# Kernel optimization log

Hardware: AMD Instinct MI355X
Metric: run time of the kernel (lower is better)

The kernel has to match this reference:

```python
import jax, jax.numpy as jnp
import numpy as np

B, N, D, H, CH = 16, 2048, 2, 128, 32
NEG = -1e9


def setup_inputs() -> dict:
    key = jax.random.key(0)
    ks = jax.random.split(key, 24)
    u = lambda k, shape, fan_in: jax.random.uniform(k, shape, jnp.float32,
                                                    -1.0 / np.sqrt(fan_in), 1.0 / np.sqrt(fan_in))
    inp = {
        "features": jax.random.normal(ks[0], (B, N, D), jnp.float32),
        "adj": jax.random.randint(ks[1], (B, N, N), 0, 2, jnp.int32),
        "candidates": jax.random.randint(ks[2], (B, N), 0, 2, jnp.int32).at[:, 0].set(1),
        "action": jnp.zeros((B,), jnp.int32),
        # GCN encoder (3 layers)
        "W1": u(ks[3], (D, H), D), "b1": jnp.zeros((H,), jnp.float32),
        "W2": u(ks[4], (H, H), H), "b2": jnp.zeros((H,), jnp.float32),
        "W3": u(ks[5], (H, H), H), "b3": jnp.zeros((H,), jnp.float32),
        # learned machine state
        "machine_state": jax.random.uniform(ks[6], (H,), jnp.float32, -1.0, 1.0),
        # actor MLP: Linear(3H,H) -> ReLU -> Linear(H,H) -> ReLU -> Linear(H,1)
        "A1": u(ks[7], (3 * H, H), 3 * H), "ab1": u(ks[8], (H,), 3 * H),
        "A2": u(ks[9], (H, H), H), "ab2": u(ks[10], (H,), H),
        "A3": u(ks[11], (H, 1), H), "ab3": u(ks[12], (1,), H),
        # critic MLP: Linear(H,CH) -> ReLU -> Linear(CH,1)
        "C1": u(ks[13], (H, CH), H), "cb1": u(ks[14], (CH,), H),
        "C2": u(ks[15], (CH, 1), CH), "cb2": u(ks[16], (1,), CH),
    }
    return inp


def _gcn_propagation_matrix(adj):
    # Faithful to PyG GCNConv(add_self_loops=True) fed edges from dense_to_sparse
    # with edge attrs discarded (all weights 1).
    A = (adj != 0).astype(jnp.float32)                      # (B,N,N), A[b,j,i]: edge j->i
    A = jnp.maximum(A, jnp.eye(N, dtype=jnp.float32))       # add_remaining_self_loops
    deg = A.sum(axis=1)                                     # (B,N) incoming degree per target i
    dis = jax.lax.rsqrt(deg)                                # deg >= 1 due to self loops
    # S[b,j,i] = dis[j] * A[j,i] * dis[i]
    return dis[:, :, None] * A * dis[:, None, :]


def reference(features, adj, candidates, action,
              W1, b1, W2, b2, W3, b3, machine_state,
              A1, ab1, A2, ab2, A3, ab3, C1, cb1, C2, cb2):
    S = _gcn_propagation_matrix(adj)
    h = features
    for W, b in ((W1, b1), (W2, b2), (W3, b3)):
        # out[b,i,:] = sum_j S[b,j,i] * (h W)[b,j,:]
        h = jax.nn.relu(jnp.einsum('bji,bjd->bid', S, h @ W) + b)
    pool = h.mean(axis=1)                                   # (B,H) global mean pool

    concat = jnp.concatenate(
        [h,
         jnp.broadcast_to(pool[:, None, :], h.shape),
         jnp.broadcast_to(machine_state[None, None, :], h.shape)], axis=-1)  # (B,N,3H)
    a = jax.nn.relu(concat @ A1 + ab1)
    a = jax.nn.relu(a @ A2 + ab2)
    scores = ((a @ A3 + ab3)[..., 0]) * 10.0                # (B,N)

    probs_sm = jax.nn.softmax(scores, axis=1)               # softmax over jobs
    logits = jnp.where(candidates != 0, probs_sm, NEG)      # masked_fill(~candidates, -inf)
    logp = jax.nn.log_softmax(logits, axis=1)               # Categorical(logits=...)
    log_prob = jnp.take_along_axis(logp, action[:, None].astype(jnp.int32), axis=1)[:, 0]
    p = jnp.exp(logp)
    entropy = -(p * logp).sum(axis=1)

    value = jax.nn.relu(pool @ C1 + cb1) @ C2 + cb2         # (B,1)
    return action, log_prob, entropy, value
```

## Files before the change

### kernel.cpp

```cpp
#include <hip/hip_runtime.h>
#include <hip/hip_bf16.h>
#include <stdint.h>

#define B_  16
#define N_  2048
#define D_  2
#define H_  128
#define CH_ 32
#define NEG_ (-1e9f)

typedef __attribute__((ext_vector_type(8))) short bf16x8;
typedef __attribute__((ext_vector_type(4))) float f32x4;
typedef unsigned short u16;

__device__ inline u16 f2bf(float f){
    union { __hip_bfloat16 h; u16 u; } cv;
    cv.h = __float2bfloat16(f);
    return cv.u;
}
__device__ inline float bf2f(u16 v){ return __uint_as_float(((unsigned)v) << 16); }

__device__ inline void gld16(const u16* g, u16* l){
    __builtin_amdgcn_global_load_lds(
        (const __attribute__((address_space(1))) unsigned int*)(const void*)g,
        (__attribute__((address_space(3))) unsigned int*)(void*)l, 16, 0, 0);
}

__global__ __launch_bounds__(256) void k_prep(const int* __restrict__ adj,
                                              u16* __restrict__ ATbf,
                                              float* __restrict__ degF){
    int i0 = blockIdx.x * 64, j0 = blockIdx.y * 64, b = blockIdx.z;
    __shared__ u16 tile[64 * 72];
    __shared__ float degP[256];
    int t = threadIdx.x;
    const int* ap = adj + (size_t)b * N_ * N_;
    #pragma unroll
    for (int it = 0; it < 4; ++it){
        int jj = it * 16 + (t >> 4);
        int gi0 = (t & 15) * 4;
        int4 a4 = *(const int4*)&ap[(size_t)(j0 + jj) * N_ + i0 + gi0];
        int gj = j0 + jj;
        tile[(gi0 + 0) * 72 + jj] = (a4.x != 0 || gj == i0 + gi0 + 0) ? (u16)0x3F80 : (u16)0;
        tile[(gi0 + 1) * 72 + jj] = (a4.y != 0 || gj == i0 + gi0 + 1) ? (u16)0x3F80 : (u16)0;
        tile[(gi0 + 2) * 72 + jj] = (a4.z != 0 || gj == i0 + gi0 + 2) ? (u16)0x3F80 : (u16)0;
        tile[(gi0 + 3) * 72 + jj] = (a4.w != 0 || gj == i0 + gi0 + 3) ? (u16)0x3F80 : (u16)0;
    }
    __syncthreads();
    {
        int ii = t & 63, q = t >> 6;
        float s = 0.f;
        #pragma unroll
        for (int k = 0; k < 16; ++k) s += (tile[ii * 72 + q * 16 + k] ? 1.f : 0.f);
        degP[t] = s;
    }
    __syncthreads();
    if (t < 64){
        float s = degP[t] + degP[t + 64] + degP[t + 128] + degP[t + 192];
        atomicAdd(&degF[b * N_ + i0 + t], s);
    }
    u16* op = ATbf + (size_t)b * N_ * N_;
    #pragma unroll
    for (int it = 0; it < 2; ++it){
        int idx = it * 256 + t;
        int io = idx >> 3, jo = (idx & 7) * 8;
        *(uint4*)&op[(size_t)(i0 + io) * N_ + j0 + jo] = *(const uint4*)&tile[io * 72 + jo];
    }
}

__global__ __launch_bounds__(256) void k_misc(const float* __restrict__ degF,
                                              float* __restrict__ dis,
                                              const float* __restrict__ W2, u16* __restrict__ WT2,
                                              const float* __restrict__ W3, u16* __restrict__ WT3,
                                              const float* __restrict__ A1, u16* __restrict__ A1aT,
                                              const float* __restrict__ A2, u16* __restrict__ A2T){
    int bx = blockIdx.x;
    if (bx < 128){
        int i = bx * 256 + threadIdx.x;
        dis[i] = rsqrtf(degF[i]);
        return;
    }
    int q = (bx - 128) >> 6;
    const float* s; u16* d;
    switch (q){
        case 0: s = W2; d = WT2; break;
        case 1: s = W3; d = WT3; break;
        case 2: s = A1; d = A1aT; break;
        default: s = A2; d = A2T; break;
    }
    int idx = ((bx - 128) & 63) * 256 + threadIdx.x;
    int hp = idx >> 7, k = idx & 127;
    d[hp * 128 + k] = f2bf(s[k * 128 + hp]);
}

__global__ __launch_bounds__(256) void k_y1(const float* __restrict__ feat,
                                            const float* __restrict__ W1,
                                            const float* __restrict__ dis,
                                            u16* __restrict__ YT){
    int j = blockIdx.x * 256 + threadIdx.x;
    int h = blockIdx.y, b = blockIdx.z;
    float f0 = feat[((size_t)b * N_ + j) * D_ + 0];
    float f1 = feat[((size_t)b * N_ + j) * D_ + 1];
    float v = dis[b * N_ + j] * (f0 * W1[h] + f1 * W1[H_ + h]);
    YT[(size_t)b * H_ * N_ + (size_t)h * N_ + j] = f2bf(v);
}

template<int MODE>
__global__ __launch_bounds__(256, 2) void k_layer(const u16* __restrict__ ATbf,
                                                  const u16* __restrict__ Yin,
                                                  const float* __restrict__ dis,
                                                  const float* __restrict__ bias,
                                                  const u16* __restrict__ WT,
                                                  u16* __restrict__ Yout,
                                                  u16* __restrict__ h3,
                                                  float* __restrict__ poolF){
    int bid = blockIdx.x;
    int b = bid & 15, i0 = (bid >> 4) * 64;
    const u16* Ab = ATbf + (size_t)b * N_ * N_ + (size_t)i0 * N_;
    const u16* Bb = Yin  + (size_t)b * H_ * N_;
    __shared__ __align__(16) u16 As[64 * 64];
    __shared__ __align__(16) u16 Bs[128 * 64];
    __shared__ __align__(16) u16 Hs[64 * 136];
    __shared__ __align__(16) u16 Ws[MODE == 0 ? 128 * 136 : 16];
    int t = threadIdx.x, w = t >> 6, lane = t & 63, quad = lane >> 4, l16 = lane & 15;
    int mr = w & 1, nc = w >> 1;
    int srow = lane >> 3;
    int xcol = ((lane & 7) ^ srow) * 8;
    int x7 = l16 & 7;

    if (MODE == 0){
        #pragma unroll
        for (int it = 0; it < 8; ++it){
            int e = it * 256 + t;
            int row = e >> 4, c8 = e & 15;
            *(uint4*)&Ws[row * 136 + c8 * 8] = *(const uint4*)&WT[row * 128 + c8 * 8];
        }
    }

    f32x4 acc[2][4];
    #pragma unroll
    for (int mt = 0; mt < 2; ++mt)
        #pragma unroll
        for (int nt = 0; nt < 4; ++nt) acc[mt][nt] = (f32x4){0.f, 0.f, 0.f, 0.f};

    for (int k0 = 0; k0 < N_; k0 += 64){
        #pragma unroll
        for (int it = 0; it < 6; ++it){
            int chunk = w * 6 + it;
            if (chunk < 8)
                gld16(Ab + (size_t)(chunk * 8 + srow) * N_ + k0 + xcol, As + chunk * 512);
            else
                gld16(Bb + (size_t)((chunk - 8) * 8 + srow) * N_ + k0 + xcol, Bs + (chunk - 8) * 512);
        }
        __syncthreads();
        #pragma unroll
        for (int kc = 0; kc < 2; ++kc){
            int gx = ((kc * 4 + quad) ^ x7) * 8;
            bf16x8 af[2];
            #pragma unroll
            for (int mt = 0; mt < 2; ++mt)
                af[mt] = *(const bf16x8*)&As[(mr * 32 + mt * 16 + l16) * 64 + gx];
            #pragma unroll
            for (int nt = 0; nt < 4; ++nt){
                bf16x8 bv = *(const bf16x8*)&Bs[(nc * 64 + nt * 16 + l16) * 64 + gx];
                #pragma unroll
                for (int mt = 0; mt < 2; ++mt)
                    acc[mt][nt] = __builtin_amdgcn_mfma_f32_16x16x32_bf16(af[mt], bv, acc[mt][nt], 0, 0, 0);
            }
        }
        __syncthreads();
    }

    #pragma unroll
    for (int mt = 0; mt < 2; ++mt)
        #pragma unroll
        for (int r = 0; r < 4; ++r){
            int m = mr * 32 + mt * 16 + quad * 4 + r;
            float dsc = dis[b * N_ + i0 + m];
            #pragma unroll
            for (int nt = 0; nt < 4; ++nt){
                int n = nc * 64 + nt * 16 + l16;
                float v = dsc * acc[mt][nt][r] + bias[n];
                Hs[m * 136 + n] = f2bf(v > 0.f ? v : 0.f);
            }
        }
    __syncthreads();

    if (MODE == 0){
        f32x4 a2[2][4];
        #pragma unroll
        for (int mt = 0; mt < 2; ++mt)
            #pragma unroll
            for (int nt = 0; nt < 4; ++nt) a2[mt][nt] = (f32x4){0.f, 0.f, 0.f, 0.f};
        #pragma unroll
        for (int kc = 0; kc < 4; ++kc){
            bf16x8 af[2];
            #pragma unroll
            for (int mt = 0; mt < 2; ++mt)
                af[mt] = *(const bf16x8*)&Hs[(mr * 32 + mt * 16 + l16) * 136 + kc * 32 + quad * 8];
            #pragma unroll
            for (int nt = 0; nt < 4; ++nt){
                bf16x8 bv = *(const bf16x8*)&Ws[(nc * 64 + nt * 16 + l16) * 136 + kc * 32 + quad * 8];
                #pragma unroll
                for (int mt = 0; mt < 2; ++mt)
                    a2[mt][nt] = __builtin_amdgcn_mfma_f32_16x16x32_bf16(af[mt], bv, a2[mt][nt], 0, 0, 0);
            }
        }
        __syncthreads();
        #pragma unroll
        for (int mt = 0; mt < 2; ++mt)
            #pragma unroll
            for (int r = 0; r < 4; ++r){
                int m = mr * 32 + mt * 16 + quad * 4 + r;
                float dsc = dis[b * N_ + i0 + m];
                #pragma unroll
                for (int nt = 0; nt < 4; ++nt)
                    Hs[m * 136 + nc * 64 + nt * 16 + l16] = f2bf(dsc * a2[mt][nt][r]);
            }
        __syncthreads();
        size_t obase = (size_t)b * H_ * N_ + i0;
        int j = t & 63, hq = t >> 6;
        #pragma unroll 8
        for (int rep = 0; rep < 32; ++rep){
            int hrow = hq * 32 + rep;
            Yout[obase + (size_t)hrow * N_ + j] = Hs[j * 136 + hrow];
        }
    } else {
        #pragma unroll
        for (int rep = 0; rep < 4; ++rep){
            int e = rep * 256 + t;
            int row = e >> 4, c8 = e & 15;
            *(uint4*)&h3[((size_t)b * N_ + i0 + row) * H_ + c8 * 8] = *(const uint4*)&Hs[row * 136 + c8 * 8];
        }
        __shared__ float pred[256];
        int n = t & 127, rq = t >> 7;
        float ps = 0.f;
        #pragma unroll 8
        for (int r = 0; r < 32; ++r) ps += bf2f(Hs[(rq * 32 + r) * 136 + n]);
        pred[t] = ps;
        __syncthreads();
        if (t < 128)
            atomicAdd(&poolF[b * H_ + t], (pred[t] + pred[t + 128]) * (1.f / N_));
    }
}

__global__ __launch_bounds__(256) void k_cv(const float* __restrict__ poolF,
                                            const float* __restrict__ ms,
                                            const float* __restrict__ A1,
                                            const float* __restrict__ ab1,
                                            const float* __restrict__ C1,
                                            const float* __restrict__ cb1,
                                            const float* __restrict__ C2,
                                            const float* __restrict__ cb2,
                                            float* __restrict__ cvec,
                                            float* __restrict__ out){
    int b = blockIdx.x, t = threadIdx.x;
    __shared__ float pl[128], msl[128], v1[32];
    if (t < 128){ pl[t] = poolF[b * H_ + t]; msl[t] = ms[t]; }
    __syncthreads();
    if (t < 128){
        float c = ab1[t];
        for (int k = 0; k < 128; ++k)
            c += pl[k] * A1[(128 + k) * H_ + t] + msl[k] * A1[(256 + k) * H_ + t];
        cvec[b * H_ + t] = c;
    } else if (t < 160){
        int cc = t - 128;
        float v = cb1[cc];
        for (int k = 0; k < 128; ++k) v += pl[k] * C1[k * CH_ + cc];
        v1[cc] = v > 0.f ? v : 0.f;
    }
    __syncthreads();
    if (t == 0){
        float v = cb2[0];
        for (int c = 0; c < CH_; ++c) v += v1[c] * C2[c];
        out[48 + b] = v;
    }
}

__global__ __launch_bounds__(256) void k_actor(const u16* __restrict__ h3,
                                               const u16* __restrict__ A1aT,
                                               const u16* __restrict__ A2T,
                                               const float* __restrict__ cvec,
                                               const float* __restrict__ ab2,
                                               const float* __restrict__ A3,
                                               const float* __restrict__ ab3,
                                               float* __restrict__ scores){
    int b = blockIdx.x, i0 = blockIdx.y * 128;
    const u16* Ab = h3 + ((size_t)b * N_ + i0) * H_;
    __shared__ __align__(16) u16 As[128 * 72];
    __shared__ __align__(16) u16 Bs[128 * 72];
    __shared__ __align__(16) u16 M1[128 * 136];
    __shared__ float sLDS[128];
    int t = threadIdx.x, w = t >> 6, lane = t & 63, quad = lane >> 4, l16 = lane & 15;
    int sr = t >> 3, sc = (t & 7) * 8;
    f32x4 acc[2][8];
    #pragma unroll
    for (int mt = 0; mt < 2; ++mt)
        #pragma unroll
        for (int nt = 0; nt < 8; ++nt) acc[mt][nt] = (f32x4){0.f, 0.f, 0.f, 0.f};
    for (int k0 = 0; k0 < H_; k0 += 64){
        #pragma unroll
        for (int it = 0; it < 4; ++it){
            int r = sr + it * 32;
            *(uint4*)&As[r * 72 + sc] = *(const uint4*)&Ab[(size_t)r * H_ + k0 + sc];
            *(uint4*)&Bs[r * 72 + sc] = *(const uint4*)&A1aT[(size_t)r * H_ + k0 + sc];
        }
        __syncthreads();
        #pragma unroll
        for (int kc = 0; kc < 2; ++kc){
            bf16x8 af[2];
            #pragma unroll
            for (int mt = 0; mt < 2; ++mt)
                af[mt] = *(const bf16x8*)&As[(w * 32 + mt * 16 + l16) * 72 + kc * 32 + quad * 8];
            #pragma unroll
            for (int nt = 0; nt < 8; ++nt){
                bf16x8 bfr = *(const bf16x8*)&Bs[(nt * 16 + l16) * 72 + kc * 32 + quad * 8];
                #pragma unroll
                for (int mt = 0; mt < 2; ++mt)
                    acc[mt][nt] = __builtin_amdgcn_mfma_f32_16x16x32_bf16(af[mt], bfr, acc[mt][nt], 0, 0, 0);
            }
        }
        __syncthreads();
    }
    const float* cv = cvec + b * H_;
    #pragma unroll
    for (int mt = 0; mt < 2; ++mt)
        #pragma unroll
        for (int r = 0; r < 4; ++r){
            int m = w * 32 + mt * 16 + quad * 4 + r;
            #pragma unroll
            for (int nt = 0; nt < 8; ++nt){
                int n = nt * 16 + l16;
                float v = acc[mt][nt][r] + cv[n];
                M1[m * 136 + n] = f2bf(v > 0.f ? v : 0.f);
                acc[mt][nt][r] = 0.f;
            }
        }
    if (t < 128) sLDS[t] = 0.f;
    for (int k0 = 0; k0 < H_; k0 += 64){
        #pragma unroll
        for (int it = 0; it < 4; ++it){
            int r = sr + it * 32;
            *(uint4*)&Bs[r * 72 + sc] = *(const uint4*)&A2T[(size_t)r * H_ + k0 + sc];
        }
        __syncthreads();
        #pragma unroll
        for (int kc = 0; kc < 2; ++kc){
            bf16x8 af[2];
            #pragma unroll
            for (int mt = 0; mt < 2; ++mt)
                af[mt] = *(const bf16x8*)&M1[(w * 32 + mt * 16 + l16) * 136 + k0 + kc * 32 + quad * 8];
            #pragma unroll
            for (int nt = 0; nt < 8; ++nt){
                bf16x8 bfr = *(const bf16x8*)&Bs[(nt * 16 + l16) * 72 + kc * 32 + quad * 8];
                #pragma unroll
                for (int mt = 0; mt < 2; ++mt)
                    acc[mt][nt] = __builtin_amdgcn_mfma_f32_16x16x32_bf16(af[mt], bfr, acc[mt][nt], 0, 0, 0);
            }
        }
        __syncthreads();
    }
    #pragma unroll
    for (int mt = 0; mt < 2; ++mt)
        #pragma unroll
        for (int r = 0; r < 4; ++r){
            int m = w * 32 + mt * 16 + quad * 4 + r;
            float part = 0.f;
            #pragma unroll
            for (int nt = 0; nt < 8; ++nt){
                int n = nt * 16 + l16;
                float v = acc[mt][nt][r] + ab2[n];
                v = v > 0.f ? v : 0.f;
                part += v * A3[n];
            }
            atomicAdd(&sLDS[m], part);
        }
    __syncthreads();
    if (t < 128) scores[(size_t)b * N_ + i0 + t] = (sLDS[t] + ab3[0]) * 10.f;
}

__device__ inline float wredS(float v){
    #pragma unroll
    for (int o = 32; o; o >>= 1) v += __shfl_xor(v, o, 64);
    return v;
}
__device__ inline float wredM(float v){
    #pragma unroll
    for (int o = 32; o; o >>= 1) v = fmaxf(v, __shfl_xor(v, o, 64));
    return v;
}

__global__ __launch_bounds__(256) void k_sm(const float* __restrict__ scores,
                                            const int* __restrict__ cand,
                                            const int* __restrict__ action,
                                            float* __restrict__ out){
    int b = blockIdx.x, t = threadIdx.x;
    __shared__ float sc[N_];
    __shared__ float red[4];
    __shared__ float lps;
    const float* sp = scores + (size_t)b * N_;
    const int*   cp = cand   + (size_t)b * N_;
    float mx = -1e30f;
    for (int i = t; i < N_; i += 256){ float v = sp[i]; sc[i] = v; mx = fmaxf(mx, v); }
    mx = wredM(mx);
    if ((t & 63) == 0) red[t >> 6] = mx;
    __syncthreads();
    mx = fmaxf(fmaxf(red[0], red[1]), fmaxf(red[2], red[3]));
    __syncthreads();
    float se = 0.f;
    for (int i = t; i < N_; i += 256) se += expf(sc[i] - mx);
    se = wredS(se);
    if ((t & 63) == 0) red[t >> 6] = se;
    __syncthreads();
    float s1 = red[0] + red[1] + red[2] + red[3];
    __syncthreads();
    float inv = 1.f / s1;
    float m2 = -1e30f;
    for (int i = t; i < N_; i += 256){
        float p = expf(sc[i] - mx) * inv;
        sc[i] = p;
        if (cp[i] != 0) m2 = fmaxf(m2, p);
    }
    m2 = wredM(m2);
    if ((t & 63) == 0) red[t >> 6] = m2;
    __syncthreads();
    m2 = fmaxf(fmaxf(red[0], red[1]), fmaxf(red[2], red[3]));
    __syncthreads();
    float s2 = 0.f;
    for (int i = t; i < N_; i += 256) if (cp[i] != 0) s2 += expf(sc[i] - m2);
    s2 = wredS(s2);
    if ((t & 63) == 0) red[t >> 6] = s2;
    __syncthreads();
    float lse = m2 + logf(red[0] + red[1] + red[2] + red[3]);
    __syncthreads();
    int a = action[b];
    float ent = 0.f;
    for (int i = t; i < N_; i += 256){
        float lp = (cp[i] != 0 ? sc[i] : NEG_) - lse;
        float pe = expf(lp);
        ent -= pe * lp;
        if (i == a) lps = lp;
    }
    ent = wredS(ent);
    if ((t & 63) == 0) red[t >> 6] = ent;
    __syncthreads();
    if (t == 0){
        out[b]      = (float)a;
        out[16 + b] = lps;
        out[32 + b] = red[0] + red[1] + red[2] + red[3];
    }
}

extern "C" void kernel_launch(void* const* d_in, const int* in_sizes, int n_in,
                              void* d_out, int out_size, void* d_ws, size_t ws_size,
                              hipStream_t stream) {
    const float* feat = (const float*)d_in[0];
    const int*   adj  = (const int*)d_in[1];
    const int*   cand = (const int*)d_in[2];
    const int*   act  = (const int*)d_in[3];
    const float* W1   = (const float*)d_in[4];
    const float* b1   = (const float*)d_in[5];
    const float* W2   = (const float*)d_in[6];
    const float* b2   = (const float*)d_in[7];
    const float* W3   = (const float*)d_in[8];
    const float* b3   = (const float*)d_in[9];
    const float* ms   = (const float*)d_in[10];
    const float* A1   = (const float*)d_in[11];
    const float* ab1  = (const float*)d_in[12];
    const float* A2   = (const float*)d_in[13];
    const float* ab2  = (const float*)d_in[14];
    const float* A3   = (const float*)d_in[15];
    const float* ab3  = (const float*)d_in[16];
    const float* C1   = (const float*)d_in[17];
    const float* cb1  = (const float*)d_in[18];
    const float* C2   = (const float*)d_in[19];
    const float* cb2  = (const float*)d_in[20];
    float* out = (float*)d_out;

    char* w8 = (char*)d_ws;
    size_t off = 0;
    auto alloc = [&](size_t bytes){ void* p = w8 + off; off += (bytes + 255) & ~(size_t)255; return p; };
    u16*   ATbf  = (u16*)  alloc((size_t)B_ * N_ * N_ * 2);
    u16*   YTa   = (u16*)  alloc((size_t)B_ * H_ * N_ * 2);
    u16*   YTb   = (u16*)  alloc((size_t)B_ * H_ * N_ * 2);
    u16*   hbuf  = (u16*)  alloc((size_t)B_ * N_ * H_ * 2);
    float* degF  = (float*)alloc((size_t)B_ * N_ * 4);
    float* poolF = (float*)alloc((size_t)B_ * H_ * 4);
    float* dis   = (float*)alloc((size_t)B_ * N_ * 4);
    float* cvec  = (float*)alloc((size_t)B_ * H_ * 4);
    float* scr   = (float*)alloc((size_t)B_ * N_ * 4);
    u16*   WT2   = (u16*)  alloc((size_t)H_ * H_ * 2);
    u16*   WT3   = (u16*)  alloc((size_t)H_ * H_ * 2);
    u16*   A1aT  = (u16*)  alloc((size_t)H_ * H_ * 2);
    u16*   A2T   = (u16*)  alloc((size_t)H_ * H_ * 2);

    hipMemsetAsync(degF, 0, (size_t)B_ * N_ * 4 + (size_t)B_ * H_ * 4, stream);

    k_prep<<<dim3(32, 32, 16), 256, 0, stream>>>(adj, ATbf, degF);
    k_misc<<<dim3(384), 256, 0, stream>>>(degF, dis, W2, WT2, W3, WT3, A1, A1aT, A2, A2T);
    k_y1  <<<dim3(8, 128, 16), 256, 0, stream>>>(feat, W1, dis, YTa);

    k_layer<0><<<dim3(512), 256, 0, stream>>>(ATbf, YTa, dis, b1, WT2, YTb, nullptr, nullptr);
    k_layer<0><<<dim3(512), 256, 0, stream>>>(ATbf, YTb, dis, b2, WT3, YTa, nullptr, nullptr);
    k_layer<1><<<dim3(512), 256, 0, stream>>>(ATbf, YTa, dis, b3, nullptr, nullptr, hbuf, poolF);

    k_cv  <<<dim3(16), 256, 0, stream>>>(poolF, ms, A1, ab1, C1, cb1, C2, cb2, cvec, out);
    k_actor<<<dim3(16, 16), 256, 0, stream>>>(hbuf, A1aT, A2T, cvec, ab2, A3, ab3, scr);
    k_sm  <<<dim3(16), 256, 0, stream>>>(scr, cand, act, out);
}
```

Measured before the change: 582.7 us.

## Quantize adjacency and node features to int8 and use i8 MFMA for GCN

Stores the 0/1 propagation matrix as int8 instead of bf16, which halves the dominant adjacency traffic. Node features are quantized per batch to int8 using an absolute-max scale that is tracked with atomicMax, and the aggregation GEMMs run on int32-accumulating i8 MFMA with dequantization in the epilogue. This adds extra quantization kernels and a bf16 staging pass. It also introduces per-batch quantization error in the features, which may affect accuracy tolerance.

Result: faster. 561.7 us (-3.6%).

```diff
diff --git a/kernel.cpp b/kernel.cpp
--- a/kernel.cpp
+++ b/kernel.cpp
@@ -11,7 +11,9 @@
 
 typedef __attribute__((ext_vector_type(8))) short bf16x8;
 typedef __attribute__((ext_vector_type(4))) float f32x4;
+typedef __attribute__((ext_vector_type(4))) int   v4i;
 typedef unsigned short u16;
+typedef signed char    i8;
 
 __device__ inline u16 f2bf(float f){
     union { __hip_bfloat16 h; u16 u; } cv;
@@ -20,17 +22,28 @@
 }
 __device__ inline float bf2f(u16 v){ return __uint_as_float(((unsigned)v) << 16); }
 
-__device__ inline void gld16(const u16* g, u16* l){
+__device__ inline void gld16b(const void* g, void* l){
     __builtin_amdgcn_global_load_lds(
-        (const __attribute__((address_space(1))) unsigned int*)(const void*)g,
-        (__attribute__((address_space(3))) unsigned int*)(void*)l, 16, 0, 0);
+        (const __attribute__((address_space(1))) unsigned int*)g,
+        (__attribute__((address_space(3))) unsigned int*)l, 16, 0, 0);
+}
+
+__device__ inline float wredS(float v){
+    #pragma unroll
+    for (int o = 32; o; o >>= 1) v += __shfl_xor(v, o, 64);
+    return v;
+}
+__device__ inline float wredM(float v){
+    #pragma unroll
+    for (int o = 32; o; o >>= 1) v = fmaxf(v, __shfl_xor(v, o, 64));
+    return v;
 }
 
 __global__ __launch_bounds__(256) void k_prep(const int* __restrict__ adj,
-                                              u16* __restrict__ ATbf,
+                                              i8* __restrict__ ATi8,
                                               float* __restrict__ degF){
     int i0 = blockIdx.x * 64, j0 = blockIdx.y * 64, b = blockIdx.z;
-    __shared__ u16 tile[64 * 72];
+    __shared__ i8 tile[64 * 80];
     __shared__ float degP[256];
     int t = threadIdx.x;
     const int* ap = adj + (size_t)b * N_ * N_;
@@ -40,17 +53,17 @@
         int gi0 = (t & 15) * 4;
         int4 a4 = *(const int4*)&ap[(size_t)(j0 + jj) * N_ + i0 + gi0];
         int gj = j0 + jj;
-        tile[(gi0 + 0) * 72 + jj] = (a4.x != 0 || gj == i0 + gi0 + 0) ? (u16)0x3F80 : (u16)0;
-        tile[(gi0 + 1) * 72 + jj] = (a4.y != 0 || gj == i0 + gi0 + 1) ? (u16)0x3F80 : (u16)0;
-        tile[(gi0 + 2) * 72 + jj] = (a4.z != 0 || gj == i0 + gi0 + 2) ? (u16)0x3F80 : (u16)0;
-        tile[(gi0 + 3) * 72 + jj] = (a4.w != 0 || gj == i0 + gi0 + 3) ? (u16)0x3F80 : (u16)0;
+        tile[(gi0 + 0) * 80 + jj] = (a4.x != 0 || gj == i0 + gi0 + 0) ? 1 : 0;
+        tile[(gi0 + 1) * 80 + jj] = (a4.y != 0 || gj == i0 + gi0 + 1) ? 1 : 0;
+        tile[(gi0 + 2) * 80 + jj] = (a4.z != 0 || gj == i0 + gi0 + 2) ? 1 : 0;
+        tile[(gi0 + 3) * 80 + jj] = (a4.w != 0 || gj == i0 + gi0 + 3) ? 1 : 0;
     }
     __syncthreads();
     {
         int ii = t & 63, q = t >> 6;
         float s = 0.f;
         #pragma unroll
-        for (int k = 0; k < 16; ++k) s += (tile[ii * 72 + q * 16 + k] ? 1.f : 0.f);
+        for (int k = 0; k < 16; ++k) s += (float)tile[ii * 80 + q * 16 + k];
         degP[t] = s;
     }
     __syncthreads();
@@ -58,12 +71,10 @@
         float s = degP[t] + degP[t + 64] + degP[t + 128] + degP[t + 192];
         atomicAdd(&degF[b * N_ + i0 + t], s);
     }
-    u16* op = ATbf + (size_t)b * N_ * N_;
-    #pragma unroll
-    for (int it = 0; it < 2; ++it){
-        int idx = it * 256 + t;
-        int io = idx >> 3, jo = (idx & 7) * 8;
-        *(uint4*)&op[(size_t)(i0 + io) * N_ + j0 + jo] = *(const uint4*)&tile[io * 72 + jo];
+    i8* op = ATi8 + (size_t)b * N_ * N_;
+    {
+        int io = t >> 2, slot = (t & 3) * 16;
+        *(uint4*)&op[(size_t)(i0 + io) * N_ + j0 + slot] = *(const uint4*)&tile[io * 80 + slot];
     }
 }
 
@@ -95,37 +106,78 @@
 __global__ __launch_bounds__(256) void k_y1(const float* __restrict__ feat,
                                             const float* __restrict__ W1,
                                             const float* __restrict__ dis,
-                                            u16* __restrict__ YT){
-    int j = blockIdx.x * 256 + threadIdx.x;
-    int h = blockIdx.y, b = blockIdx.z;
+                                            u16* __restrict__ YT,
+                                            int* __restrict__ absm){
+    int t = threadIdx.x;
+    int j = blockIdx.x * 256 + t;
+    int hg = blockIdx.y * 8;
+    int b = blockIdx.z;
     float f0 = feat[((size_t)b * N_ + j) * D_ + 0];
     float f1 = feat[((size_t)b * N_ + j) * D_ + 1];
-    float v = dis[b * N_ + j] * (f0 * W1[h] + f1 * W1[H_ + h]);
-    YT[(size_t)b * H_ * N_ + (size_t)h * N_ + j] = f2bf(v);
+    float dsc = dis[b * N_ + j];
+    float lm = 0.f;
+    #pragma unroll
+    for (int hh = 0; hh < 8; ++hh){
+        int h = hg + hh;
+        float v = dsc * (f0 * W1[h] + f1 * W1[H_ + h]);
+        lm = fmaxf(lm, fabsf(v));
+        YT[(size_t)b * H_ * N_ + (size_t)h * N_ + j] = f2bf(v);
+    }
+    __shared__ float rmax[256];
+    rmax[t] = lm;
+    __syncthreads();
+    if (t < 128) rmax[t] = fmaxf(rmax[t], rmax[t + 128]);
+    __syncthreads();
+    if (t < 64){
+        float mv = wredM(fmaxf(rmax[t], rmax[t + 64]));
+        if (t == 0) atomicMax(&absm[b], __float_as_int(mv));
+    }
+}
+
+__global__ __launch_bounds__(256) void k_quant(const u16* __restrict__ Yb,
+                                               const int* __restrict__ absm,
+                                               i8* __restrict__ Yq){
+    int idx = (blockIdx.x * 256 + threadIdx.x) * 8;
+    int b = idx >> 18;
+    float am = __int_as_float(absm[b]);
+    float s = (am > 0.f) ? 126.f / am : 0.f;
+    bf16x8 y = *(const bf16x8*)&Yb[idx];
+    int q[8];
+    #pragma unroll
+    for (int e = 0; e < 8; ++e){
+        float f = bf2f((u16)y[e]) * s;
+        q[e] = (int)rintf(f);
+    }
+    unsigned lo = (q[0] & 255) | ((q[1] & 255) << 8) | ((q[2] & 255) << 16) | ((unsigned)(q[3] & 255) << 24);
+    unsigned hi = (q[4] & 255) | ((q[5] & 255) << 8) | ((q[6] & 255) << 16) | ((unsigned)(q[7] & 255) << 24);
+    *(uint2*)&Yq[idx] = make_uint2(lo, hi);
 }
 
 template<int MODE>
-__global__ __launch_bounds__(256, 2) void k_layer(const u16* __restrict__ ATbf,
-                                                  const u16* __restrict__ Yin,
+__global__ __launch_bounds__(256, 2) void k_layer(const i8* __restrict__ ATi8,
+                                                  const i8* __restrict__ Yq,
                                                   const float* __restrict__ dis,
                                                   const float* __restrict__ bias,
+                                                  const int* __restrict__ absmIn,
                                                   const u16* __restrict__ WT,
                                                   u16* __restrict__ Yout,
+                                                  int* __restrict__ absmOut,
                                                   u16* __restrict__ h3,
                                                   float* __restrict__ poolF){
     int bid = blockIdx.x;
     int b = bid & 15, i0 = (bid >> 4) * 64;
-    const u16* Ab = ATbf + (size_t)b * N_ * N_ + (size_t)i0 * N_;
-    const u16* Bb = Yin  + (size_t)b * H_ * N_;
-    __shared__ __align__(16) u16 As[64 * 64];
-    __shared__ __align__(16) u16 Bs[128 * 64];
+    const i8* Ab = ATi8 + (size_t)b * N_ * N_ + (size_t)i0 * N_;
+    const i8* Bb = Yq   + (size_t)b * H_ * N_;
+    __shared__ __align__(16) i8 As[64 * 64];
+    __shared__ __align__(16) i8 Bs[128 * 64];
     __shared__ __align__(16) u16 Hs[64 * 136];
     __shared__ __align__(16) u16 Ws[MODE == 0 ? 128 * 136 : 16];
+    __shared__ float pmax[256];
     int t = threadIdx.x, w = t >> 6, lane = t & 63, quad = lane >> 4, l16 = lane & 15;
     int mr = w & 1, nc = w >> 1;
-    int srow = lane >> 3;
-    int xcol = ((lane & 7) ^ srow) * 8;
-    int x7 = l16 & 7;
+
+    float am = __int_as_float(absmIn[b]);
+    float inv_s = am * (1.f / 126.f);
 
     if (MODE == 0){
         #pragma unroll
@@ -136,36 +188,36 @@
         }
     }
 
-    f32x4 acc[2][4];
+    v4i acc[2][4];
     #pragma unroll
     for (int mt = 0; mt < 2; ++mt)
         #pragma unroll
-        for (int nt = 0; nt < 4; ++nt) acc[mt][nt] = (f32x4){0.f, 0.f, 0.f, 0.f};
+        for (int nt = 0; nt < 4; ++nt) acc[mt][nt] = (v4i){0, 0, 0, 0};
+
+    int srow = lane & 15;
+    int sslot = ((lane >> 4) ^ (lane & 3)) * 16;
+    int fxo = (quad ^ (l16 & 3)) * 256 + l16 * 16;
 
     for (int k0 = 0; k0 < N_; k0 += 64){
         #pragma unroll
-        for (int it = 0; it < 6; ++it){
-            int chunk = w * 6 + it;
-            if (chunk < 8)
-                gld16(Ab + (size_t)(chunk * 8 + srow) * N_ + k0 + xcol, As + chunk * 512);
+        for (int it = 0; it < 3; ++it){
+            int g = w * 3 + it;
+            if (g < 4)
+                gld16b(Ab + (size_t)(g * 16 + srow) * N_ + k0 + sslot, As + g * 1024);
             else
-                gld16(Bb + (size_t)((chunk - 8) * 8 + srow) * N_ + k0 + xcol, Bs + (chunk - 8) * 512);
-        }
-        __syncthreads();
-        #pragma unroll
-        for (int kc = 0; kc < 2; ++kc){
-            int gx = ((kc * 4 + quad) ^ x7) * 8;
-            bf16x8 af[2];
+                gld16b(Bb + (size_t)((g - 4) * 16 + srow) * N_ + k0 + sslot, Bs + (g - 4) * 1024);
+        }
+        __syncthreads();
+        v4i af[2];
+        #pragma unroll
+        for (int mt = 0; mt < 2; ++mt)
+            af[mt] = *(const v4i*)&As[(mr * 2 + mt) * 1024 + fxo];
+        #pragma unroll
+        for (int nt = 0; nt < 4; ++nt){
+            v4i bv = *(const v4i*)&Bs[(nc * 4 + nt) * 1024 + fxo];
             #pragma unroll
             for (int mt = 0; mt < 2; ++mt)
-                af[mt] = *(const bf16x8*)&As[(mr * 32 + mt * 16 + l16) * 64 + gx];
-            #pragma unroll
-            for (int nt = 0; nt < 4; ++nt){
-                bf16x8 bv = *(const bf16x8*)&Bs[(nc * 64 + nt * 16 + l16) * 64 + gx];
-                #pragma unroll
-                for (int mt = 0; mt < 2; ++mt)
-                    acc[mt][nt] = __builtin_amdgcn_mfma_f32_16x16x32_bf16(af[mt], bv, acc[mt][nt], 0, 0, 0);
-            }
+                acc[mt][nt] = __builtin_amdgcn_mfma_i32_16x16x64_i8(af[mt], bv, acc[mt][nt], 0, 0, 0);
         }
         __syncthreads();
     }
@@ -179,7 +231,7 @@
             #pragma unroll
             for (int nt = 0; nt < 4; ++nt){
                 int n = nc * 64 + nt * 16 + l16;
-                float v = dsc * acc[mt][nt][r] + bias[n];
+                float v = dsc * ((float)acc[mt][nt][r] * inv_s) + bias[n];
                 Hs[m * 136 + n] = f2bf(v > 0.f ? v : 0.f);
             }
         }
@@ -206,6 +258,7 @@
             }
         }
         __syncthreads();
+        float lmax = 0.f;
         #pragma unroll
         for (int mt = 0; mt < 2; ++mt)
             #pragma unroll
@@ -213,9 +266,13 @@
                 int m = mr * 32 + mt * 16 + quad * 4 + r;
                 float dsc = dis[b * N_ + i0 + m];
                 #pragma unroll
-                for (int nt = 0; nt < 4; ++nt)
-                    Hs[m * 136 + nc * 64 + nt * 16 + l16] = f2bf(dsc * a2[mt][nt][r]);
-            }
+                for (int nt = 0; nt < 4; ++nt){
+                    float v = dsc * a2[mt][nt][r];
+                    lmax = fmaxf(lmax, fabsf(v));
+                    Hs[m * 136 + nc * 64 + nt * 16 + l16] = f2bf(v);
+                }
+            }
+        pmax[t] = lmax;
         __syncthreads();
         size_t obase = (size_t)b * H_ * N_ + i0;
         int j = t & 63, hq = t >> 6;
@@ -224,6 +281,11 @@
             int hrow = hq * 32 + rep;
             Yout[obase + (size_t)hrow * N_ + j] = Hs[j * 136 + hrow];
         }
+        if (t < 64){
+            float mv = fmaxf(fmaxf(pmax[t], pmax[t + 64]), fmaxf(pmax[t + 128], pmax[t + 192]));
+            mv = wredM(mv);
+            if (t == 0) atomicMax(&absmOut[b], __float_as_int(mv));
+        }
     } else {
         #pragma unroll
         for (int rep = 0; rep < 4; ++rep){
@@ -231,15 +293,14 @@
             int row = e >> 4, c8 = e & 15;
             *(uint4*)&h3[((size_t)b * N_ + i0 + row) * H_ + c8 * 8] = *(const uint4*)&Hs[row * 136 + c8 * 8];
         }
-        __shared__ float pred[256];
         int n = t & 127, rq = t >> 7;
         float ps = 0.f;
         #pragma unroll 8
         for (int r = 0; r < 32; ++r) ps += bf2f(Hs[(rq * 32 + r) * 136 + n]);
-        pred[t] = ps;
+        pmax[t] = ps;
         __syncthreads();
         if (t < 128)
-            atomicAdd(&poolF[b * H_ + t], (pred[t] + pred[t + 128]) * (1.f / N_));
+            atomicAdd(&poolF[b * H_ + t], (pmax[t] + pmax[t + 128]) * (1.f / N_));
     }
 }
 
@@ -376,17 +437,6 @@
         }
     __syncthreads();
     if (t < 128) scores[(size_t)b * N_ + i0 + t] = (sLDS[t] + ab3[0]) * 10.f;
-}
-
-__device__ inline float wredS(float v){
-    #pragma unroll
-    for (int o = 32; o; o >>= 1) v += __shfl_xor(v, o, 64);
-    return v;
-}
-__device__ inline float wredM(float v){
-    #pragma unroll
-    for (int o = 32; o; o >>= 1) v = fmaxf(v, __shfl_xor(v, o, 64));
-    return v;
 }
 
 __global__ __launch_bounds__(256) void k_sm(const float* __restrict__ scores,
@@ -479,12 +529,14 @@
     char* w8 = (char*)d_ws;
     size_t off = 0;
     auto alloc = [&](size_t bytes){ void* p = w8 + off; off += (bytes + 255) & ~(size_t)255; return p; };
-    u16*   ATbf  = (u16*)  alloc((size_t)B_ * N_ * N_ * 2);
-    u16*   YTa   = (u16*)  alloc((size_t)B_ * H_ * N_ * 2);
-    u16*   YTb   = (u16*)  alloc((size_t)B_ * H_ * N_ * 2);
+    i8*    ATi8  = (i8*)   alloc((size_t)B_ * N_ * N_);
+    u16*   Yb16  = (u16*)  alloc((size_t)B_ * H_ * N_ * 2);
+    i8*    Yi8A  = (i8*)   alloc((size_t)B_ * H_ * N_);
+    i8*    Yi8B  = (i8*)   alloc((size_t)B_ * H_ * N_);
     u16*   hbuf  = (u16*)  alloc((size_t)B_ * N_ * H_ * 2);
     float* degF  = (float*)alloc((size_t)B_ * N_ * 4);
     float* poolF = (float*)alloc((size_t)B_ * H_ * 4);
+    int*   absm  = (int*)  alloc(48 * 4);
     float* dis   = (float*)alloc((size_t)B_ * N_ * 4);
     float* cvec  = (float*)alloc((size_t)B_ * H_ * 4);
     float* scr   = (float*)alloc((size_t)B_ * N_ * 4);
@@ -493,15 +545,18 @@
     u16*   A1aT  = (u16*)  alloc((size_t)H_ * H_ * 2);
     u16*   A2T   = (u16*)  alloc((size_t)H_ * H_ * 2);
 
-    hipMemsetAsync(degF, 0, (size_t)B_ * N_ * 4 + (size_t)B_ * H_ * 4, stream);
-
-    k_prep<<<dim3(32, 32, 16), 256, 0, stream>>>(adj, ATbf, degF);
+    hipMemsetAsync(degF, 0, (size_t)B_ * N_ * 4 + (size_t)B_ * H_ * 4 + 256, stream);
+
+    k_prep<<<dim3(32, 32, 16), 256, 0, stream>>>(adj, ATi8, degF);
     k_misc<<<dim3(384), 256, 0, stream>>>(degF, dis, W2, WT2, W3, WT3, A1, A1aT, A2, A2T);
-    k_y1  <<<dim3(8, 128, 16), 256, 0, stream>>>(feat, W1, dis, YTa);
-
-    k_layer<0><<<dim3(512), 256, 0, stream>>>(ATbf, YTa, dis, b1, WT2, YTb, nullptr, nullptr);
-    k_layer<0><<<dim3(512), 256, 0, stream>>>(ATbf, YTb, dis, b2, WT3, YTa, nullptr, nullptr);
-    k_layer<1><<<dim3(512), 256, 0, stream>>>(ATbf, YTa, dis, b3, nullptr, nullptr, hbuf, poolF);
+    k_y1  <<<dim3(8, 16, 16), 256, 0, stream>>>(feat, W1, dis, Yb16, absm + 0);
+    k_quant<<<dim3(2048), 256, 0, stream>>>(Yb16, absm + 0, Yi8A);
+
+    k_layer<0><<<dim3(512), 256, 0, stream>>>(ATi8, Yi8A, dis, b1, absm + 0,  WT2, Yb16, absm + 16, nullptr, nullptr);
+    k_quant<<<dim3(2048), 256, 0, stream>>>(Yb16, absm + 16, Yi8B);
+    k_layer<0><<<dim3(512), 256, 0, stream>>>(ATi8, Yi8B, dis, b2, absm + 16, WT3, Yb16, absm + 32, nullptr, nullptr);
+    k_quant<<<dim3(2048), 256, 0, stream>>>(Yb16, absm + 32, Yi8A);
+    k_layer<1><<<dim3(512), 256, 0, stream>>>(ATi8, Yi8A, dis, b3, absm + 32, nullptr, nullptr, nullptr, hbuf, poolF);
 
     k_cv  <<<dim3(16), 256, 0, stream>>>(poolF, ms, A1, ab1, C1, cb1, C2, cb2, cvec, out);
     k_actor<<<dim3(16, 16), 256, 0, stream>>>(hbuf, A1aT, A2T, cvec, ab2, A3, ab3, scr);
```
